# Performance work log

Hardware: AMD Instinct MI355X
Metric: run time of the kernel (lower is better)

## Reference

```python
import jax, jax.numpy as jnp
import numpy as np

H, DK, DV, D, K = 8, 128, 128, 1024, 4


def _dconv(x, w, b):
    # Causal depthwise conv1d (torch Conv1d groups=C, padding=K-1, sliced to seq_len)
    # x: [B,L,C], w: [C,K], b: [C]
    B, L, C = x.shape
    xp = jnp.pad(x, ((0, 0), (K - 1, 0), (0, 0)))
    acc = xp[:, 0:L, :] * w[:, 0]
    for j in range(1, K):
        acc = acc + xp[:, j:j + L, :] * w[:, j]
    return acc + b


def _forward(x, Wq, Wk, Wv, Wa, ba, Wb, bb, Wg, Wo, cqw, cqb, ckw, ckb, cvw, cvb, ln_g, ln_b):
    B, L, _ = x.shape
    q = jax.nn.silu(_dconv(x @ Wq, cqw, cqb)).reshape(B, L, H, DK)
    k = jax.nn.silu(_dconv(x @ Wk, ckw, ckb)).reshape(B, L, H, DK) * (DK ** -0.5)
    v = jax.nn.silu(_dconv(x @ Wv, cvw, cvb)).reshape(B, L, H, DV)
    a = jax.nn.sigmoid(x @ Wa + ba).reshape(B, L, H, DV)      # channel-wise decay gates
    beta = jax.nn.sigmoid(x @ Wb + bb)                         # [B,L,H] write strength

    tm = lambda t: jnp.moveaxis(t, 1, 0)  # time-major for scan

    def step(S, ins):
        # S: [B,H,DV,DK]
        qt, kt, vt, at, bt = ins
        err = jnp.einsum('bhvk,bhk->bhv', S, kt) - vt                        # delta-rule error (old state)
        Sn = at[..., None] * S - (bt[..., None, None] * err[..., None]) * kt[:, :, None, :]
        ot = jnp.einsum('bhvk,bhk->bhv', Sn, qt)                             # readout with NEW state
        return Sn, ot

    S0 = jnp.zeros((B, H, DV, DK), x.dtype)
    _, oT = jax.lax.scan(step, S0, (tm(q), tm(k), tm(v), tm(a), tm(beta)))
    o = jnp.moveaxis(oT, 0, 1)  # [B,L,H,DV]

    mu = o.mean(-1, keepdims=True)
    var = o.var(-1, keepdims=True)
    o = (o - mu) / jnp.sqrt(var + 1e-5) * ln_g + ln_b          # LayerNorm over head_dim_v

    g = jax.nn.sigmoid(x @ Wg).reshape(B, L, H, DV)
    o = (o * g).reshape(B, L, H * DV)
    return o @ Wo


def setup_inputs() -> dict:
    key = jax.random.key(0)
    ks = jax.random.split(key, 16)
    B, L = 4, 2048
    s = 0.02
    f32 = jnp.float32
    return {
        'x':   jax.random.normal(ks[0], (B, L, D), f32),
        'Wq':  jax.random.normal(ks[1], (D, H * DK), f32) * s,
        'Wk':  jax.random.normal(ks[2], (D, H * DK), f32) * s,
        'Wv':  jax.random.normal(ks[3], (D, H * DV), f32) * s,
        'Wa':  jax.random.normal(ks[4], (D, H * DV), f32) * s,
        'ba':  jnp.zeros((H * DV,), f32),
        'Wb':  jax.random.normal(ks[5], (D, H), f32) * s,
        'bb':  jnp.zeros((H,), f32),
        'Wg':  jax.random.normal(ks[6], (D, H * DV), f32) * s,
        'Wo':  jax.random.normal(ks[7], (H * DV, D), f32) * s,
        'cqw': jax.random.normal(ks[8], (H * DK, K), f32) * 0.2,
        'cqb': jnp.zeros((H * DK,), f32),
        'ckw': jax.random.normal(ks[9], (H * DK, K), f32) * 0.2,
        'ckb': jnp.zeros((H * DK,), f32),
        'cvw': jax.random.normal(ks[10], (H * DV, K), f32) * 0.2,
        'cvb': jnp.zeros((H * DV,), f32),
        'ln_g': jnp.ones((DV,), f32),
        'ln_b': jnp.zeros((DV,), f32),
    }


def reference(x, Wq, Wk, Wv, Wa, ba, Wb, bb, Wg, Wo, cqw, cqb, ckw, ckb, cvw, cvb, ln_g, ln_b):
    return _forward(x, Wq, Wk, Wv, Wa, ba, Wb, bb, Wg, Wo, cqw, cqb, ckw, ckb, cvw, cvb, ln_g, ln_b)
```

## Files before the change

### kernel.cpp

```cpp
#include <hip/hip_runtime.h>

typedef unsigned short u16;
typedef __attribute__((ext_vector_type(8))) unsigned short ushort8;
typedef __attribute__((ext_vector_type(4))) unsigned short ushort4v;
typedef __attribute__((ext_vector_type(8))) short bf16x8;
typedef __attribute__((ext_vector_type(4))) float f32x4;

#define LB    2048
#define DIM   1024
#define NCAT  5248
#define MROWS 8192
#define G     16
#define NG    (LB / G)

__device__ __forceinline__ float b2f(u16 u) {
    unsigned int x = ((unsigned int)u) << 16;
    return __builtin_bit_cast(float, x);
}
__device__ __forceinline__ u16 f2b(float f) {
    unsigned int u = __builtin_bit_cast(unsigned int, f);
    u = u + 0x7FFFu + ((u >> 16) & 1u);
    return (u16)(u >> 16);
}
__device__ __forceinline__ float sigm(float x) { return 1.0f / (1.0f + __expf(-x)); }

template <int CTRL>
__device__ __forceinline__ float dpp_addf(float x) {
    int y = __builtin_amdgcn_update_dpp(0, __builtin_bit_cast(int, x), CTRL, 0xF, 0xF, true);
    return x + __builtin_bit_cast(float, y);
}
__device__ __forceinline__ float sum8_dpp(float x) {
    x = dpp_addf<0xB1>(x);
    x = dpp_addf<0x4E>(x);
    x = dpp_addf<0x141>(x);
    return x;
}

__global__ void f32_to_bf16(const float* __restrict__ src, u16* __restrict__ dst, int n) {
    int i = (blockIdx.x * 256 + threadIdx.x) * 4;
    if (i >= n) return;
    float4 v = *(const float4*)(src + i);
    ushort4v u;
    u[0] = f2b(v.x); u[1] = f2b(v.y); u[2] = f2b(v.z); u[3] = f2b(v.w);
    *(ushort4v*)(dst + i) = u;
}

__global__ void transpose_f32_bf16(const float* __restrict__ src, u16* __restrict__ dst, int cols) {
    const int cidx = blockIdx.x;
    const int r = blockIdx.y * 256 + threadIdx.x;
    dst[(size_t)cidx * 1024 + r] = f2b(src[(size_t)r * cols + cidx]);
}

__global__ void fill_zero_u16(u16* __restrict__ dst, int n) {
    int i = blockIdx.x * 256 + threadIdx.x;
    if (i < n) dst[i] = 0;
}

template <int OUT_IS_F32>
__global__ __launch_bounds__(256) void gemm_bt(const u16* __restrict__ A,
                                               const u16* __restrict__ Bt,
                                               void* __restrict__ Cv,
                                               int M, int N, int K) {
    __shared__ u16 lds_a[128 * 40];
    __shared__ u16 lds_b[128 * 40];
    const int tid = threadIdx.x;
    const int m0 = blockIdx.y * 128;
    const int n0 = blockIdx.x * 128;
    const int w = tid >> 6;
    const int l = tid & 63;
    const int wm = w >> 1, wn = w & 1;
    const int lr = l & 15, kg = l >> 4;

    f32x4 acc[4][4];
#pragma unroll
    for (int m = 0; m < 4; ++m)
#pragma unroll
        for (int n = 0; n < 4; ++n)
            acc[m][n] = f32x4{0.f, 0.f, 0.f, 0.f};

    const int r0 = tid >> 2;
    const int cc0 = tid & 3;

    for (int kt = 0; kt < K; kt += 32) {
#pragma unroll
        for (int i = 0; i < 2; ++i) {
            const int rr = r0 + i * 64;
            ushort8 va = *(const ushort8*)(A + (size_t)(m0 + rr) * K + kt + cc0 * 8);
            ushort8 vb = *(const ushort8*)(Bt + (size_t)(n0 + rr) * K + kt + cc0 * 8);
            *(ushort8*)&lds_a[rr * 40 + cc0 * 8] = va;
            *(ushort8*)&lds_b[rr * 40 + cc0 * 8] = vb;
        }
        __syncthreads();
        bf16x8 af[4], bfv[4];
#pragma unroll
        for (int m = 0; m < 4; ++m)
            af[m] = *(const bf16x8*)&lds_a[(wm * 64 + m * 16 + lr) * 40 + kg * 8];
#pragma unroll
        for (int n = 0; n < 4; ++n)
            bfv[n] = *(const bf16x8*)&lds_b[(wn * 64 + n * 16 + lr) * 40 + kg * 8];
#pragma unroll
        for (int m = 0; m < 4; ++m)
#pragma unroll
            for (int n = 0; n < 4; ++n)
                acc[m][n] = __builtin_amdgcn_mfma_f32_16x16x32_bf16(af[m], bfv[n], acc[m][n], 0, 0, 0);
        __syncthreads();
    }

#pragma unroll
    for (int m = 0; m < 4; ++m) {
#pragma unroll
        for (int n = 0; n < 4; ++n) {
            const int col = n0 + wn * 64 + n * 16 + lr;
#pragma unroll
            for (int j = 0; j < 4; ++j) {
                const int row = m0 + wm * 64 + m * 16 + kg * 4 + j;
                if (OUT_IS_F32)
                    ((float*)Cv)[(size_t)row * N + col] = acc[m][n][j];
                else
                    ((u16*)Cv)[(size_t)row * N + col] = f2b(acc[m][n][j]);
            }
        }
    }
}

__global__ __launch_bounds__(256) void conv_silu(const u16* __restrict__ pre,
                                                 u16* __restrict__ dst,
                                                 const float* __restrict__ w,
                                                 const float* __restrict__ bias,
                                                 float scale, int col_off) {
    const int row = blockIdx.x;
    const int l = row & (LB - 1);
    const int ch = threadIdx.x * 4;
    const float4* wv = (const float4*)(w + ch * 4);
    float wt[4][4];
#pragma unroll
    for (int c = 0; c < 4; ++c) {
        float4 t = wv[c];
        wt[c][0] = t.x; wt[c][1] = t.y; wt[c][2] = t.z; wt[c][3] = t.w;
    }
    float acc[4] = {bias[ch + 0], bias[ch + 1], bias[ch + 2], bias[ch + 3]};
#pragma unroll
    for (int dd = 0; dd < 4; ++dd) {
        if (l - 3 + dd >= 0) {
            ushort4v vv = *(const ushort4v*)(pre + (size_t)(row - 3 + dd) * NCAT + col_off + ch);
#pragma unroll
            for (int c = 0; c < 4; ++c) acc[c] += b2f(vv[c]) * wt[c][dd];
        }
    }
    ushort4v outv;
#pragma unroll
    for (int c = 0; c < 4; ++c) {
        float a = acc[c];
        outv[c] = f2b(a * sigm(a) * scale);
    }
    *(ushort4v*)(dst + (size_t)row * DIM + ch) = outv;
}

__global__ __launch_bounds__(128) void scan_kernel(const u16* __restrict__ qb,
                                                   const u16* __restrict__ kb,
                                                   const u16* __restrict__ vb,
                                                   const u16* __restrict__ pre,
                                                   const float* __restrict__ ba,
                                                   const float* __restrict__ bb,
                                                   float* __restrict__ o) {
    const int bid = blockIdx.x;
    const int vc = (bid >> 3) & 7;
    const int bh = (bid & 7) * 4 + (bid >> 6);
    const int h = bh & 7;
    const int b = bh >> 3;

    const int tid = threadIdx.x;
    const int r = tid >> 3;
    const int c = tid & 7;
    const int k0 = c * 16;
    const int v0 = vc * 16;
    const size_t row0 = (size_t)b * LB;

    __shared__ u16 k_lds[2][G][128];
    __shared__ u16 q_lds[2][G][128];
    __shared__ float v_ldsf[2][G][16];
    __shared__ float a_ldsf[2][G][16];
    __shared__ float b_ldsf[2][G];

    const float bbv = bb[h];

    const int st_t = tid >> 3;
    const int st_c = tid & 7;
    const u16* kgp = kb + row0 * DIM + h * 128 + st_c * 16;
    const u16* qgp = qb + row0 * DIM + h * 128 + st_c * 16;
    const u16* vgp = vb + row0 * DIM + h * 128 + v0 + (tid & 1) * 8;
    const u16* agp = pre + row0 * NCAT + 3072 + h * 128 + v0 + (tid & 1) * 8;
    const u16* bgp = pre + row0 * NCAT + 5120 + h;
    float* op = o + row0 * DIM + h * 128 + v0 + r;

    float baf[8];
    if (tid >= 32 && tid < 64) {
        const float* bap = ba + h * 128 + v0 + (tid & 1) * 8;
#pragma unroll
        for (int j = 0; j < 8; ++j) baf[j] = bap[j];
    }

    ushort8 kst0, kst1, qst0, qst1, vst, ast;
    u16 bst;
    ushort8 kn0, kn1, qn0, qn1;
    float vnf, anf, bnf;

#define STAGE_LOAD(gl) do {                                                     \
        const size_t rk = (size_t)((gl) * G + st_t) * DIM;                      \
        kst0 = *(const ushort8*)(kgp + rk);                                     \
        kst1 = *(const ushort8*)(kgp + rk + 8);                                 \
        qst0 = *(const ushort8*)(qgp + rk);                                     \
        qst1 = *(const ushort8*)(qgp + rk + 8);                                 \
        if (tid < 32) {                                                         \
            vst = *(const ushort8*)(vgp + (size_t)((gl) * G + (tid >> 1)) * DIM); \
        } else if (tid < 64) {                                                  \
            ast = *(const ushort8*)(agp + (size_t)((gl) * G + ((tid - 32) >> 1)) * NCAT); \
        } else if (tid < 80) {                                                  \
            bst = bgp[(size_t)((gl) * G + (tid - 64)) * NCAT];                  \
        }                                                                       \
    } while (0)

#define STAGE_WRITE(bufi) do {                                                  \
        *(ushort8*)&k_lds[bufi][st_t][st_c * 16] = kst0;                        \
        *(ushort8*)&k_lds[bufi][st_t][st_c * 16 + 8] = kst1;                    \
        *(ushort8*)&q_lds[bufi][st_t][st_c * 16] = qst0;                        \
        *(ushort8*)&q_lds[bufi][st_t][st_c * 16 + 8] = qst1;                    \
        if (tid < 32) {                                                         \
            float* d = &v_ldsf[bufi][tid >> 1][(tid & 1) * 8];                  \
            _Pragma("unroll") for (int j = 0; j < 8; ++j) d[j] = b2f(vst[j]);   \
        } else if (tid < 64) {                                                  \
            float* d = &a_ldsf[bufi][(tid - 32) >> 1][(tid & 1) * 8];           \
            _Pragma("unroll") for (int j = 0; j < 8; ++j) d[j] = sigm(b2f(ast[j]) + baf[j]); \
        } else if (tid < 80) {                                                  \
            b_ldsf[bufi][tid - 64] = sigm(b2f(bst) + bbv);                      \
        }                                                                       \
    } while (0)

#define PREFETCH(bufi, tt) do {                                                 \
        kn0 = *(const ushort8*)&k_lds[bufi][tt][k0];                            \
        kn1 = *(const ushort8*)&k_lds[bufi][tt][k0 + 8];                        \
        qn0 = *(const ushort8*)&q_lds[bufi][tt][k0];                            \
        qn1 = *(const ushort8*)&q_lds[bufi][tt][k0 + 8];                        \
        vnf = v_ldsf[bufi][tt][r];                                              \
        anf = a_ldsf[bufi][tt][r];                                              \
        bnf = b_ldsf[bufi][tt];                                                 \
    } while (0)

    float S[16];
#pragma unroll
    for (int j = 0; j < 16; ++j) S[j] = 0.f;

    STAGE_LOAD(0);
    STAGE_WRITE(0);
    __syncthreads();
    PREFETCH(0, 0);

    for (int g = 0; g < NG; ++g) {
        const int buf = g & 1;
        const int gn = (g + 1 < NG) ? g + 1 : g;
        STAGE_LOAD(gn);

#pragma unroll
        for (int t = 0; t < G; ++t) {
            const ushort8 kc0 = kn0, kc1 = kn1, qc0 = qn0, qc1 = qn1;
            const float vcf = vnf, acf = anf, bcf = bnf;
            if (t < G - 1) PREFETCH(buf, t + 1);

            float kf[16], qf[16];
#pragma unroll
            for (int j = 0; j < 8; ++j) {
                kf[j] = b2f(kc0[j]); kf[8 + j] = b2f(kc1[j]);
                qf[j] = b2f(qc0[j]); qf[8 + j] = b2f(qc1[j]);
            }

            float e0 = 0.f, e1 = 0.f, e2 = 0.f, e3 = 0.f;
#pragma unroll
            for (int j = 0; j < 4; ++j) {
                e0 += S[j] * kf[j];
                e1 += S[4 + j] * kf[4 + j];
                e2 += S[8 + j] * kf[8 + j];
                e3 += S[12 + j] * kf[12 + j];
            }
            float e = sum8_dpp((e0 + e1) + (e2 + e3));
            const float be = bcf * (e - vcf);

            float p0 = 0.f, p1 = 0.f, p2 = 0.f, p3 = 0.f;
#pragma unroll
            for (int j = 0; j < 4; ++j) {
                S[j] = acf * S[j] - be * kf[j];                p0 += S[j] * qf[j];
                S[4 + j] = acf * S[4 + j] - be * kf[4 + j];    p1 += S[4 + j] * qf[4 + j];
                S[8 + j] = acf * S[8 + j] - be * kf[8 + j];    p2 += S[8 + j] * qf[8 + j];
                S[12 + j] = acf * S[12 + j] - be * kf[12 + j]; p3 += S[12 + j] * qf[12 + j];
            }
            float po = sum8_dpp((p0 + p1) + (p2 + p3));
            if (c == 0) op[(size_t)(g * G + t) * DIM] = po;
        }

        STAGE_WRITE(buf ^ 1);
        __syncthreads();
        PREFETCH(buf ^ 1, 0);
    }
#undef STAGE_LOAD
#undef STAGE_WRITE
#undef PREFETCH
}

__global__ __launch_bounds__(256) void ln_gate(const float* __restrict__ o,
                                               const u16* __restrict__ pre,
                                               const float* __restrict__ ln_g,
                                               const float* __restrict__ ln_b,
                                               u16* __restrict__ o2) {
    const int row = blockIdx.x;
    const int tid = threadIdx.x;
    const int h = tid >> 5;
    const int lg = tid & 31;
    const int d0 = lg * 4;
    float4 x = *(const float4*)(o + (size_t)row * DIM + h * 128 + d0);
    float s = x.x + x.y + x.z + x.w;
    float ss = x.x * x.x + x.y * x.y + x.z * x.z + x.w * x.w;
#pragma unroll
    for (int m = 1; m <= 16; m <<= 1) {
        s += __shfl_xor(s, m);
        ss += __shfl_xor(ss, m);
    }
    const float mu = s * (1.f / 128.f);
    const float var = ss * (1.f / 128.f) - mu * mu;
    const float inv = rsqrtf(var + 1e-5f);
    ushort4v gp = *(const ushort4v*)(pre + (size_t)row * NCAT + 4096 + h * 128 + d0);
    float4 lg4 = *(const float4*)(ln_g + d0);
    float4 lb4 = *(const float4*)(ln_b + d0);
    float xv[4] = {x.x, x.y, x.z, x.w};
    float gv[4] = {lg4.x, lg4.y, lg4.z, lg4.w};
    float bv[4] = {lb4.x, lb4.y, lb4.z, lb4.w};
    ushort4v outv;
#pragma unroll
    for (int q = 0; q < 4; ++q) {
        float y = (xv[q] - mu) * inv * gv[q] + bv[q];
        y *= sigm(b2f(gp[q]));
        outv[q] = f2b(y);
    }
    *(ushort4v*)(o2 + (size_t)row * DIM + h * 128 + d0) = outv;
}

extern "C" void kernel_launch(void* const* d_in, const int* in_sizes, int n_in,
                              void* d_out, int out_size, void* d_ws, size_t ws_size,
                              hipStream_t stream) {
    const float* x   = (const float*)d_in[0];
    const float* Wq  = (const float*)d_in[1];
    const float* Wk  = (const float*)d_in[2];
    const float* Wv  = (const float*)d_in[3];
    const float* Wa  = (const float*)d_in[4];
    const float* ba  = (const float*)d_in[5];
    const float* Wb  = (const float*)d_in[6];
    const float* bb  = (const float*)d_in[7];
    const float* Wg  = (const float*)d_in[8];
    const float* Wo  = (const float*)d_in[9];
    const float* cqw = (const float*)d_in[10];
    const float* cqb = (const float*)d_in[11];
    const float* ckw = (const float*)d_in[12];
    const float* ckb = (const float*)d_in[13];
    const float* cvw = (const float*)d_in[14];
    const float* cvb = (const float*)d_in[15];
    const float* lng = (const float*)d_in[16];
    const float* lnb = (const float*)d_in[17];

    const size_t NEED = (size_t)MROWS * DIM * 2
                      + (size_t)NCAT * DIM * 2
                      + (size_t)DIM * DIM * 2
                      + (size_t)MROWS * NCAT * 2
                      + 3 * (size_t)MROWS * DIM * 2
                      + (size_t)MROWS * DIM * 4
                      + (size_t)MROWS * DIM * 2;
    if (ws_size < NEED) return;

    char* p = (char*)d_ws;
    u16* x_bf  = (u16*)p; p += (size_t)MROWS * DIM * 2;
    u16* wcatT = (u16*)p; p += (size_t)NCAT * DIM * 2;
    u16* woT   = (u16*)p; p += (size_t)DIM * DIM * 2;
    u16* pre   = (u16*)p; p += (size_t)MROWS * NCAT * 2;
    u16* qbuf  = (u16*)p; p += (size_t)MROWS * DIM * 2;
    u16* kbuf  = (u16*)p; p += (size_t)MROWS * DIM * 2;
    u16* vbuf  = (u16*)p; p += (size_t)MROWS * DIM * 2;
    float* obuf = (float*)p; p += (size_t)MROWS * DIM * 4;
    u16* o2buf = (u16*)p;

    f32_to_bf16<<<MROWS * DIM / 1024, 256, 0, stream>>>(x, x_bf, MROWS * DIM);
    transpose_f32_bf16<<<dim3(1024, 4), 256, 0, stream>>>(Wq, wcatT + 0 * 1024 * 1024, 1024);
    transpose_f32_bf16<<<dim3(1024, 4), 256, 0, stream>>>(Wk, wcatT + 1 * 1024 * 1024, 1024);
    transpose_f32_bf16<<<dim3(1024, 4), 256, 0, stream>>>(Wv, wcatT + 2 * 1024 * 1024, 1024);
    transpose_f32_bf16<<<dim3(1024, 4), 256, 0, stream>>>(Wa, wcatT + 3 * 1024 * 1024, 1024);
    transpose_f32_bf16<<<dim3(1024, 4), 256, 0, stream>>>(Wg, wcatT + 4 * 1024 * 1024, 1024);
    transpose_f32_bf16<<<dim3(8, 4), 256, 0, stream>>>(Wb, wcatT + (size_t)5120 * 1024, 8);
    transpose_f32_bf16<<<dim3(1024, 4), 256, 0, stream>>>(Wo, woT, 1024);
    fill_zero_u16<<<(120 * 1024 + 255) / 256, 256, 0, stream>>>(wcatT + (size_t)5128 * 1024, 120 * 1024);

    gemm_bt<0><<<dim3(NCAT / 128, MROWS / 128), 256, 0, stream>>>(x_bf, wcatT, pre, MROWS, NCAT, DIM);

    conv_silu<<<MROWS, 256, 0, stream>>>(pre, qbuf, cqw, cqb, 1.0f, 0);
    conv_silu<<<MROWS, 256, 0, stream>>>(pre, kbuf, ckw, ckb, 0.08838834764831845f, 1024);
    conv_silu<<<MROWS, 256, 0, stream>>>(pre, vbuf, cvw, cvb, 1.0f, 2048);

    scan_kernel<<<256, 128, 0, stream>>>(qbuf, kbuf, vbuf, pre, ba, bb, obuf);

    ln_gate<<<MROWS, 256, 0, stream>>>(obuf, pre, lng, lnb, o2buf);

    gemm_bt<1><<<dim3(DIM / 128, MROWS / 128), 256, 0, stream>>>(o2buf, woT, d_out, MROWS, DIM, DIM);
}
```

Baseline: 1.010 ms.

## Use direct global-to-LDS loads in GEMM and double v-rows per scan thread

The GEMM tile loads now use global_load_lds to write straight into LDS, and the padded LDS stride of 40 becomes an unpadded 32, which may add bank conflicts on the MFMA fragment reads. The scan kernel gives each thread two state rows (32 v-columns per block instead of 16), which halves the grid to 128 blocks. The per-step k/q loads and conversions are now shared across twice the work and there is more ILP per step. The cost is fewer resident waves on a latency-bound recurrence and more register pressure.

```diff
diff --git a/kernel.cpp b/kernel.cpp
--- a/kernel.cpp
+++ b/kernel.cpp
@@ -34,6 +34,11 @@
     x = dpp_addf<0x4E>(x);
     x = dpp_addf<0x141>(x);
     return x;
+}
+
+__device__ __forceinline__ void gload_lds16(const u16* g, u16* l) {
+    __builtin_amdgcn_global_load_lds((const __attribute__((address_space(1))) void*)g,
+                                     (__attribute__((address_space(3))) void*)l, 16, 0, 0);
 }
 
 __global__ void f32_to_bf16(const float* __restrict__ src, u16* __restrict__ dst, int n) {
@@ -61,8 +66,8 @@
                                                const u16* __restrict__ Bt,
                                                void* __restrict__ Cv,
                                                int M, int N, int K) {
-    __shared__ u16 lds_a[128 * 40];
-    __shared__ u16 lds_b[128 * 40];
+    __shared__ u16 lds_a[128 * 32];
+    __shared__ u16 lds_b[128 * 32];
     const int tid = threadIdx.x;
     const int m0 = blockIdx.y * 128;
     const int n0 = blockIdx.x * 128;
@@ -78,26 +83,24 @@
         for (int n = 0; n < 4; ++n)
             acc[m][n] = f32x4{0.f, 0.f, 0.f, 0.f};
 
-    const int r0 = tid >> 2;
-    const int cc0 = tid & 3;
+    const int srow = (l >> 2);
+    const int scol = (l & 3) * 8;
 
     for (int kt = 0; kt < K; kt += 32) {
 #pragma unroll
-        for (int i = 0; i < 2; ++i) {
-            const int rr = r0 + i * 64;
-            ushort8 va = *(const ushort8*)(A + (size_t)(m0 + rr) * K + kt + cc0 * 8);
-            ushort8 vb = *(const ushort8*)(Bt + (size_t)(n0 + rr) * K + kt + cc0 * 8);
-            *(ushort8*)&lds_a[rr * 40 + cc0 * 8] = va;
-            *(ushort8*)&lds_b[rr * 40 + cc0 * 8] = vb;
+        for (int ld = 0; ld < 2; ++ld) {
+            const int row = w * 32 + ld * 16 + srow;
+            gload_lds16(A + (size_t)(m0 + row) * K + kt + scol, &lds_a[(w * 32 + ld * 16) * 32]);
+            gload_lds16(Bt + (size_t)(n0 + row) * K + kt + scol, &lds_b[(w * 32 + ld * 16) * 32]);
         }
         __syncthreads();
         bf16x8 af[4], bfv[4];
 #pragma unroll
         for (int m = 0; m < 4; ++m)
-            af[m] = *(const bf16x8*)&lds_a[(wm * 64 + m * 16 + lr) * 40 + kg * 8];
+            af[m] = *(const bf16x8*)&lds_a[(wm * 64 + m * 16 + lr) * 32 + kg * 8];
 #pragma unroll
         for (int n = 0; n < 4; ++n)
-            bfv[n] = *(const bf16x8*)&lds_b[(wn * 64 + n * 16 + lr) * 40 + kg * 8];
+            bfv[n] = *(const bf16x8*)&lds_b[(wn * 64 + n * 16 + lr) * 32 + kg * 8];
 #pragma unroll
         for (int m = 0; m < 4; ++m)
 #pragma unroll
@@ -164,8 +167,10 @@
                                                    const float* __restrict__ bb,
                                                    float* __restrict__ o) {
     const int bid = blockIdx.x;
-    const int vc = (bid >> 3) & 7;
-    const int bh = (bid & 7) * 4 + (bid >> 6);
+    const int xcd = bid & 7;
+    const int inner = bid >> 3;
+    const int bh = xcd * 4 + (inner >> 2);
+    const int vp = inner & 3;
     const int h = bh & 7;
     const int b = bh >> 3;
 
@@ -173,82 +178,80 @@
     const int r = tid >> 3;
     const int c = tid & 7;
     const int k0 = c * 16;
-    const int v0 = vc * 16;
+    const int v0 = vp * 32;
     const size_t row0 = (size_t)b * LB;
 
     __shared__ u16 k_lds[2][G][128];
     __shared__ u16 q_lds[2][G][128];
-    __shared__ float v_ldsf[2][G][16];
-    __shared__ float a_ldsf[2][G][16];
+    __shared__ float v_ldsf[2][G][32];
+    __shared__ float a_ldsf[2][G][32];
     __shared__ float b_ldsf[2][G];
 
     const float bbv = bb[h];
 
-    const int st_t = tid >> 3;
-    const int st_c = tid & 7;
+    const int st_t = tid >> 3, st_c = tid & 7;
     const u16* kgp = kb + row0 * DIM + h * 128 + st_c * 16;
     const u16* qgp = qb + row0 * DIM + h * 128 + st_c * 16;
-    const u16* vgp = vb + row0 * DIM + h * 128 + v0 + (tid & 1) * 8;
-    const u16* agp = pre + row0 * NCAT + 3072 + h * 128 + v0 + (tid & 1) * 8;
+    const int vt = tid >> 2, vc4 = tid & 3;
+    const u16* vgp = vb + row0 * DIM + h * 128 + v0 + vc4 * 8;
+    const int aidx = tid - 64, at = aidx >> 2, ac4 = aidx & 3;
+    const u16* agp = pre + row0 * NCAT + 3072 + h * 128 + v0 + ac4 * 8;
     const u16* bgp = pre + row0 * NCAT + 5120 + h;
     float* op = o + row0 * DIM + h * 128 + v0 + r;
 
     float baf[8];
-    if (tid >= 32 && tid < 64) {
-        const float* bap = ba + h * 128 + v0 + (tid & 1) * 8;
-#pragma unroll
-        for (int j = 0; j < 8; ++j) baf[j] = bap[j];
+    if (tid >= 64) {
+#pragma unroll
+        for (int j = 0; j < 8; ++j) baf[j] = ba[h * 128 + v0 + ac4 * 8 + j];
     }
 
     ushort8 kst0, kst1, qst0, qst1, vst, ast;
     u16 bst;
     ushort8 kn0, kn1, qn0, qn1;
-    float vnf, anf, bnf;
-
-#define STAGE_LOAD(gl) do {                                                     \
-        const size_t rk = (size_t)((gl) * G + st_t) * DIM;                      \
-        kst0 = *(const ushort8*)(kgp + rk);                                     \
-        kst1 = *(const ushort8*)(kgp + rk + 8);                                 \
-        qst0 = *(const ushort8*)(qgp + rk);                                     \
-        qst1 = *(const ushort8*)(qgp + rk + 8);                                 \
-        if (tid < 32) {                                                         \
-            vst = *(const ushort8*)(vgp + (size_t)((gl) * G + (tid >> 1)) * DIM); \
-        } else if (tid < 64) {                                                  \
-            ast = *(const ushort8*)(agp + (size_t)((gl) * G + ((tid - 32) >> 1)) * NCAT); \
-        } else if (tid < 80) {                                                  \
-            bst = bgp[(size_t)((gl) * G + (tid - 64)) * NCAT];                  \
-        }                                                                       \
+    float vAn, vBn, aAn, aBn, bnf;
+
+#define STAGE_LOAD(gl) do {                                                       \
+        const size_t rk = (size_t)((gl) * G + st_t) * DIM;                        \
+        kst0 = *(const ushort8*)(kgp + rk);                                       \
+        kst1 = *(const ushort8*)(kgp + rk + 8);                                   \
+        qst0 = *(const ushort8*)(qgp + rk);                                       \
+        qst1 = *(const ushort8*)(qgp + rk + 8);                                   \
+        if (tid < 64) {                                                           \
+            vst = *(const ushort8*)(vgp + (size_t)((gl) * G + vt) * DIM);         \
+        } else {                                                                  \
+            ast = *(const ushort8*)(agp + (size_t)((gl) * G + at) * NCAT);        \
+        }                                                                         \
+        if (tid < 16) bst = bgp[(size_t)((gl) * G + tid) * NCAT];                 \
     } while (0)
 
-#define STAGE_WRITE(bufi) do {                                                  \
-        *(ushort8*)&k_lds[bufi][st_t][st_c * 16] = kst0;                        \
-        *(ushort8*)&k_lds[bufi][st_t][st_c * 16 + 8] = kst1;                    \
-        *(ushort8*)&q_lds[bufi][st_t][st_c * 16] = qst0;                        \
-        *(ushort8*)&q_lds[bufi][st_t][st_c * 16 + 8] = qst1;                    \
-        if (tid < 32) {                                                         \
-            float* d = &v_ldsf[bufi][tid >> 1][(tid & 1) * 8];                  \
-            _Pragma("unroll") for (int j = 0; j < 8; ++j) d[j] = b2f(vst[j]);   \
-        } else if (tid < 64) {                                                  \
-            float* d = &a_ldsf[bufi][(tid - 32) >> 1][(tid & 1) * 8];           \
+#define STAGE_WRITE(bufi) do {                                                    \
+        *(ushort8*)&k_lds[bufi][st_t][st_c * 16] = kst0;                          \
+        *(ushort8*)&k_lds[bufi][st_t][st_c * 16 + 8] = kst1;                      \
+        *(ushort8*)&q_lds[bufi][st_t][st_c * 16] = qst0;                          \
+        *(ushort8*)&q_lds[bufi][st_t][st_c * 16 + 8] = qst1;                      \
+        if (tid < 64) {                                                           \
+            float* d = &v_ldsf[bufi][vt][vc4 * 8];                                \
+            _Pragma("unroll") for (int j = 0; j < 8; ++j) d[j] = b2f(vst[j]);     \
+        } else {                                                                  \
+            float* d = &a_ldsf[bufi][at][ac4 * 8];                                \
             _Pragma("unroll") for (int j = 0; j < 8; ++j) d[j] = sigm(b2f(ast[j]) + baf[j]); \
-        } else if (tid < 80) {                                                  \
-            b_ldsf[bufi][tid - 64] = sigm(b2f(bst) + bbv);                      \
-        }                                                                       \
+        }                                                                         \
+        if (tid < 16) b_ldsf[bufi][tid] = sigm(b2f(bst) + bbv);                   \
     } while (0)
 
-#define PREFETCH(bufi, tt) do {                                                 \
-        kn0 = *(const ushort8*)&k_lds[bufi][tt][k0];                            \
-        kn1 = *(const ushort8*)&k_lds[bufi][tt][k0 + 8];                        \
-        qn0 = *(const ushort8*)&q_lds[bufi][tt][k0];                            \
-        qn1 = *(const ushort8*)&q_lds[bufi][tt][k0 + 8];                        \
-        vnf = v_ldsf[bufi][tt][r];                                              \
-        anf = a_ldsf[bufi][tt][r];                                              \
-        bnf = b_ldsf[bufi][tt];                                                 \
+#define PREFETCH(bufi, tt) do {                                                   \
+        kn0 = *(const ushort8*)&k_lds[bufi][tt][k0];                              \
+        kn1 = *(const ushort8*)&k_lds[bufi][tt][k0 + 8];                          \
+        qn0 = *(const ushort8*)&q_lds[bufi][tt][k0];                              \
+        qn1 = *(const ushort8*)&q_lds[bufi][tt][k0 + 8];                          \
+        vAn = v_ldsf[bufi][tt][r];  vBn = v_ldsf[bufi][tt][16 + r];               \
+        aAn = a_ldsf[bufi][tt][r];  aBn = a_ldsf[bufi][tt][16 + r];               \
+        bnf = b_ldsf[bufi][tt];                                                   \
     } while (0)
 
-    float S[16];
-#pragma unroll
-    for (int j = 0; j < 16; ++j) S[j] = 0.f;
+    float SA[16], SB[16];
+#pragma unroll
+    for (int j = 0; j < 16; ++j) { SA[j] = 0.f; SB[j] = 0.f; }
 
     STAGE_LOAD(0);
     STAGE_WRITE(0);
@@ -263,7 +266,7 @@
 #pragma unroll
         for (int t = 0; t < G; ++t) {
             const ushort8 kc0 = kn0, kc1 = kn1, qc0 = qn0, qc1 = qn1;
-            const float vcf = vnf, acf = anf, bcf = bnf;
+            const float vA = vAn, vB = vBn, aA = aAn, aB = aBn, bt_ = bnf;
             if (t < G - 1) PREFETCH(buf, t + 1);
 
             float kf[16], qf[16];
@@ -273,27 +276,39 @@
                 qf[j] = b2f(qc0[j]); qf[8 + j] = b2f(qc1[j]);
             }
 
-            float e0 = 0.f, e1 = 0.f, e2 = 0.f, e3 = 0.f;
+            float eA0 = 0.f, eA1 = 0.f, eA2 = 0.f, eA3 = 0.f;
+            float eB0 = 0.f, eB1 = 0.f, eB2 = 0.f, eB3 = 0.f;
 #pragma unroll
             for (int j = 0; j < 4; ++j) {
-                e0 += S[j] * kf[j];
-                e1 += S[4 + j] * kf[4 + j];
-                e2 += S[8 + j] * kf[8 + j];
-                e3 += S[12 + j] * kf[12 + j];
+                eA0 += SA[j] * kf[j];           eB0 += SB[j] * kf[j];
+                eA1 += SA[4 + j] * kf[4 + j];   eB1 += SB[4 + j] * kf[4 + j];
+                eA2 += SA[8 + j] * kf[8 + j];   eB2 += SB[8 + j] * kf[8 + j];
+                eA3 += SA[12 + j] * kf[12 + j]; eB3 += SB[12 + j] * kf[12 + j];
             }
-            float e = sum8_dpp((e0 + e1) + (e2 + e3));
-            const float be = bcf * (e - vcf);
-
-            float p0 = 0.f, p1 = 0.f, p2 = 0.f, p3 = 0.f;
+            float eA = sum8_dpp((eA0 + eA1) + (eA2 + eA3));
+            float eB = sum8_dpp((eB0 + eB1) + (eB2 + eB3));
+            const float beA = bt_ * (eA - vA);
+            const float beB = bt_ * (eB - vB);
+
+            float pA0 = 0.f, pA1 = 0.f, pA2 = 0.f, pA3 = 0.f;
+            float pB0 = 0.f, pB1 = 0.f, pB2 = 0.f, pB3 = 0.f;
 #pragma unroll
             for (int j = 0; j < 4; ++j) {
-                S[j] = acf * S[j] - be * kf[j];                p0 += S[j] * qf[j];
-                S[4 + j] = acf * S[4 + j] - be * kf[4 + j];    p1 += S[4 + j] * qf[4 + j];
-                S[8 + j] = acf * S[8 + j] - be * kf[8 + j];    p2 += S[8 + j] * qf[8 + j];
-                S[12 + j] = acf * S[12 + j] - be * kf[12 + j]; p3 += S[12 + j] * qf[12 + j];
+                SA[j] = aA * SA[j] - beA * kf[j];                 pA0 += SA[j] * qf[j];
+                SB[j] = aB * SB[j] - beB * kf[j];                 pB0 += SB[j] * qf[j];
+                SA[4 + j] = aA * SA[4 + j] - beA * kf[4 + j];     pA1 += SA[4 + j] * qf[4 + j];
+                SB[4 + j] = aB * SB[4 + j] - beB * kf[4 + j];     pB1 += SB[4 + j] * qf[4 + j];
+                SA[8 + j] = aA * SA[8 + j] - beA * kf[8 + j];     pA2 += SA[8 + j] * qf[8 + j];
+                SB[8 + j] = aB * SB[8 + j] - beB * kf[8 + j];     pB2 += SB[8 + j] * qf[8 + j];
+                SA[12 + j] = aA * SA[12 + j] - beA * kf[12 + j];  pA3 += SA[12 + j] * qf[12 + j];
+                SB[12 + j] = aB * SB[12 + j] - beB * kf[12 + j];  pB3 += SB[12 + j] * qf[12 + j];
             }
-            float po = sum8_dpp((p0 + p1) + (p2 + p3));
-            if (c == 0) op[(size_t)(g * G + t) * DIM] = po;
+            float poA = sum8_dpp((pA0 + pA1) + (pA2 + pA3));
+            float poB = sum8_dpp((pB0 + pB1) + (pB2 + pB3));
+            if (c == 0) {
+                op[(size_t)(g * G + t) * DIM] = poA;
+                op[(size_t)(g * G + t) * DIM + 16] = poB;
+            }
         }
 
         STAGE_WRITE(buf ^ 1);
@@ -400,7 +415,7 @@
     conv_silu<<<MROWS, 256, 0, stream>>>(pre, kbuf, ckw, ckb, 0.08838834764831845f, 1024);
     conv_silu<<<MROWS, 256, 0, stream>>>(pre, vbuf, cvw, cvb, 1.0f, 2048);
 
-    scan_kernel<<<256, 128, 0, stream>>>(qbuf, kbuf, vbuf, pre, ba, bb, obuf);
+    scan_kernel<<<128, 128, 0, stream>>>(qbuf, kbuf, vbuf, pre, ba, bb, obuf);
 
     ln_gate<<<MROWS, 256, 0, stream>>>(obuf, pre, lng, lnb, o2buf);
 
```

Result: slower. 1.225 ms (+21.3%).

## Use direct global-to-LDS loads in GEMM and deepen scan LDS prefetch

Applied to the files above, without the earlier changes.

The GEMM tile staging now uses global_load_lds to copy A/B tiles straight into shared memory, skipping the register round trip. Because this path writes contiguously, the padded row stride of 40 becomes an unpadded stride of 32. The recurrent scan kernel now prefetches k/q/v/a/beta from LDS four timesteps ahead in a ring of register slots instead of one, to hide LDS latency on the serial dependency chain. Risks are more LDS bank conflicts from dropping the padding, and higher register pressure in the scan kernel.

```diff
diff --git a/kernel.cpp b/kernel.cpp
--- a/kernel.cpp
+++ b/kernel.cpp
@@ -34,6 +34,11 @@
     x = dpp_addf<0x4E>(x);
     x = dpp_addf<0x141>(x);
     return x;
+}
+
+__device__ __forceinline__ void gload_lds16(const u16* g, u16* l) {
+    __builtin_amdgcn_global_load_lds((const __attribute__((address_space(1))) void*)g,
+                                     (__attribute__((address_space(3))) void*)l, 16, 0, 0);
 }
 
 __global__ void f32_to_bf16(const float* __restrict__ src, u16* __restrict__ dst, int n) {
@@ -61,8 +66,8 @@
                                                const u16* __restrict__ Bt,
                                                void* __restrict__ Cv,
                                                int M, int N, int K) {
-    __shared__ u16 lds_a[128 * 40];
-    __shared__ u16 lds_b[128 * 40];
+    __shared__ u16 lds_a[128 * 32];
+    __shared__ u16 lds_b[128 * 32];
     const int tid = threadIdx.x;
     const int m0 = blockIdx.y * 128;
     const int n0 = blockIdx.x * 128;
@@ -78,26 +83,25 @@
         for (int n = 0; n < 4; ++n)
             acc[m][n] = f32x4{0.f, 0.f, 0.f, 0.f};
 
-    const int r0 = tid >> 2;
-    const int cc0 = tid & 3;
+    const int srow = (l >> 2);
+    const int scol = (l & 3) * 8;
+    (void)srow;
 
     for (int kt = 0; kt < K; kt += 32) {
 #pragma unroll
-        for (int i = 0; i < 2; ++i) {
-            const int rr = r0 + i * 64;
-            ushort8 va = *(const ushort8*)(A + (size_t)(m0 + rr) * K + kt + cc0 * 8);
-            ushort8 vb = *(const ushort8*)(Bt + (size_t)(n0 + rr) * K + kt + cc0 * 8);
-            *(ushort8*)&lds_a[rr * 40 + cc0 * 8] = va;
-            *(ushort8*)&lds_b[rr * 40 + cc0 * 8] = vb;
+        for (int ld = 0; ld < 2; ++ld) {
+            const int row = w * 32 + ld * 16 + (l >> 2);
+            gload_lds16(A + (size_t)(m0 + row) * K + kt + scol, &lds_a[(w * 32 + ld * 16) * 32]);
+            gload_lds16(Bt + (size_t)(n0 + row) * K + kt + scol, &lds_b[(w * 32 + ld * 16) * 32]);
         }
         __syncthreads();
         bf16x8 af[4], bfv[4];
 #pragma unroll
         for (int m = 0; m < 4; ++m)
-            af[m] = *(const bf16x8*)&lds_a[(wm * 64 + m * 16 + lr) * 40 + kg * 8];
+            af[m] = *(const bf16x8*)&lds_a[(wm * 64 + m * 16 + lr) * 32 + kg * 8];
 #pragma unroll
         for (int n = 0; n < 4; ++n)
-            bfv[n] = *(const bf16x8*)&lds_b[(wn * 64 + n * 16 + lr) * 40 + kg * 8];
+            bfv[n] = *(const bf16x8*)&lds_b[(wn * 64 + n * 16 + lr) * 32 + kg * 8];
 #pragma unroll
         for (int m = 0; m < 4; ++m)
 #pragma unroll
@@ -202,8 +206,9 @@
 
     ushort8 kst0, kst1, qst0, qst1, vst, ast;
     u16 bst;
-    ushort8 kn0, kn1, qn0, qn1;
-    float vnf, anf, bnf;
+
+    ushort8 kpf0[4], kpf1[4], qpf0[4], qpf1[4];
+    float vpf[4], apf[4], bpf[4];
 
 #define STAGE_LOAD(gl) do {                                                     \
         const size_t rk = (size_t)((gl) * G + st_t) * DIM;                      \
@@ -236,14 +241,14 @@
         }                                                                       \
     } while (0)
 
-#define PREFETCH(bufi, tt) do {                                                 \
-        kn0 = *(const ushort8*)&k_lds[bufi][tt][k0];                            \
-        kn1 = *(const ushort8*)&k_lds[bufi][tt][k0 + 8];                        \
-        qn0 = *(const ushort8*)&q_lds[bufi][tt][k0];                            \
-        qn1 = *(const ushort8*)&q_lds[bufi][tt][k0 + 8];                        \
-        vnf = v_ldsf[bufi][tt][r];                                              \
-        anf = a_ldsf[bufi][tt][r];                                              \
-        bnf = b_ldsf[bufi][tt];                                                 \
+#define PREF(bufi, tt, sl) do {                                                 \
+        kpf0[sl] = *(const ushort8*)&k_lds[bufi][tt][k0];                       \
+        kpf1[sl] = *(const ushort8*)&k_lds[bufi][tt][k0 + 8];                   \
+        qpf0[sl] = *(const ushort8*)&q_lds[bufi][tt][k0];                       \
+        qpf1[sl] = *(const ushort8*)&q_lds[bufi][tt][k0 + 8];                   \
+        vpf[sl] = v_ldsf[bufi][tt][r];                                          \
+        apf[sl] = a_ldsf[bufi][tt][r];                                          \
+        bpf[sl] = b_ldsf[bufi][tt];                                             \
     } while (0)
 
     float S[16];
@@ -253,7 +258,7 @@
     STAGE_LOAD(0);
     STAGE_WRITE(0);
     __syncthreads();
-    PREFETCH(0, 0);
+    PREF(0, 0, 0); PREF(0, 1, 1); PREF(0, 2, 2); PREF(0, 3, 3);
 
     for (int g = 0; g < NG; ++g) {
         const int buf = g & 1;
@@ -262,16 +267,19 @@
 
 #pragma unroll
         for (int t = 0; t < G; ++t) {
-            const ushort8 kc0 = kn0, kc1 = kn1, qc0 = qn0, qc1 = qn1;
-            const float vcf = vnf, acf = anf, bcf = bnf;
-            if (t < G - 1) PREFETCH(buf, t + 1);
+            const int sl = t & 3;
 
             float kf[16], qf[16];
 #pragma unroll
             for (int j = 0; j < 8; ++j) {
-                kf[j] = b2f(kc0[j]); kf[8 + j] = b2f(kc1[j]);
-                qf[j] = b2f(qc0[j]); qf[8 + j] = b2f(qc1[j]);
+                kf[j] = b2f(kpf0[sl][j]); kf[8 + j] = b2f(kpf1[sl][j]);
+                qf[j] = b2f(qpf0[sl][j]); qf[8 + j] = b2f(qpf1[sl][j]);
             }
+            const float vcf = vpf[sl];
+            const float acf = apf[sl];
+            const float bcf = bpf[sl];
+
+            if (t < G - 4) PREF(buf, t + 4, sl);
 
             float e0 = 0.f, e1 = 0.f, e2 = 0.f, e3 = 0.f;
 #pragma unroll
@@ -298,11 +306,12 @@
 
         STAGE_WRITE(buf ^ 1);
         __syncthreads();
-        PREFETCH(buf ^ 1, 0);
+        const int nb = buf ^ 1;
+        PREF(nb, 0, 0); PREF(nb, 1, 1); PREF(nb, 2, 2); PREF(nb, 3, 3);
     }
 #undef STAGE_LOAD
 #undef STAGE_WRITE
-#undef PREFETCH
+#undef PREF
 }
 
 __global__ __launch_bounds__(256) void ln_gate(const float* __restrict__ o,
```

Measured after the change: 979.6 us. 1.03x faster.
